# Kernel tuning notes

Hardware: AMD Instinct MI355X
Metric: run time of the kernel (lower is better)

## Reference

```python
import jax, jax.numpy as jnp
import numpy as np

EPS = 1e-5

def mlp_layer(h, W, b, g, be):
    # Linear -> BatchNorm1d (training-mode batch stats over points) -> LeakyReLU
    y = h @ W + b
    mu = jnp.mean(y, axis=0)
    var = jnp.mean((y - mu) ** 2, axis=0)
    y = (y - mu) * jax.lax.rsqrt(var + EPS) * g + be
    return jax.nn.leaky_relu(y, 0.01)

def segment_unit_norm(pos, idx, S):
    # center each segment on its centroid, scale to the unit sphere, return radius*2 as diameter
    N = pos.shape[0]
    cnt = jax.ops.segment_sum(jnp.ones((N,), pos.dtype), idx, num_segments=S)
    center = jax.ops.segment_sum(pos, idx, num_segments=S) / jnp.maximum(cnt, 1.0)[:, None]
    centered = pos - center[idx]
    r2 = jax.ops.segment_max(jnp.sum(centered * centered, axis=1), idx, num_segments=S)
    r = jnp.sqrt(jnp.maximum(r2, 0.0))  # empty segments -> -inf clamped to 0
    r_safe = jnp.where(r > 0.0, r, 1.0)
    pos_n = centered / r_safe[idx][:, None]
    diameter = 2.0 * r_safe * (cnt > 0).astype(pos.dtype)
    return pos_n, diameter, cnt

def segment_max_pool(x, idx, S, cnt):
    out = jax.ops.segment_max(x, idx, num_segments=S)
    return jnp.where((cnt > 0)[:, None], out, 0.0)

def setup_inputs() -> dict:
    key = jax.random.key(0)
    ks = jax.random.split(key, 16)
    N, S = 1000000, 10000
    Cx = 64
    loc = [Cx + 3, 128, 256]
    glo = [loc[-1] + 1, 512, 512]
    d = {
        'pos': jax.random.normal(ks[0], (N, 3), jnp.float32),
        'x': jax.random.normal(ks[1], (N, Cx), jnp.float32),
        'idx': jnp.sort(jax.random.randint(ks[2], (N,), 0, S)),
        'num_segments': S,
    }
    def lin(k, fan_in, fan_out):
        s = 1.0 / np.sqrt(fan_in)
        return jax.random.uniform(k, (fan_in, fan_out), jnp.float32, -s, s)
    # local MLP params
    d['W1'], d['b1'] = lin(ks[3], loc[0], loc[1]), jnp.zeros((loc[1],), jnp.float32)
    d['g1'], d['be1'] = jnp.ones((loc[1],), jnp.float32), jnp.zeros((loc[1],), jnp.float32)
    d['W2'], d['b2'] = lin(ks[4], loc[1], loc[2]), jnp.zeros((loc[2],), jnp.float32)
    d['g2'], d['be2'] = jnp.ones((loc[2],), jnp.float32), jnp.zeros((loc[2],), jnp.float32)
    # global MLP params
    d['GW1'], d['Gb1'] = lin(ks[5], glo[0], glo[1]), jnp.zeros((glo[1],), jnp.float32)
    d['Gg1'], d['Gbe1'] = jnp.ones((glo[1],), jnp.float32), jnp.zeros((glo[1],), jnp.float32)
    d['GW2'], d['Gb2'] = lin(ks[6], glo[1], glo[2]), jnp.zeros((glo[2],), jnp.float32)
    d['Gg2'], d['Gbe2'] = jnp.ones((glo[2],), jnp.float32), jnp.zeros((glo[2],), jnp.float32)
    return d

def reference(pos, x, idx, num_segments, W1, b1, g1, be1, W2, b2, g2, be2, GW1, Gb1, Gg1, Gbe1, GW2, Gb2, Gg2, Gbe2):
    S = num_segments
    pos_n, diameter, cnt = segment_unit_norm(pos, idx, S)
    h = jnp.concatenate([x, pos_n], axis=1)            # [N, 67]
    h = mlp_layer(h, W1, b1, g1, be1)                   # [N, 128]
    h = mlp_layer(h, W2, b2, g2, be2)                   # [N, 256]
    hg = segment_max_pool(h, idx, S, cnt)               # [S, 256]
    hg = jnp.concatenate([hg, diameter[:, None]], axis=1)  # [S, 257]
    hg = mlp_layer(hg, GW1, Gb1, Gg1, Gbe1)             # [S, 512]
    hg = mlp_layer(hg, GW2, Gb2, Gg2, Gbe2)             # [S, 512]
    return hg
```

## Files before the change

kernel.cpp:

```cpp
#include <hip/hip_runtime.h>
#include <hip/hip_fp16.h>

#define LEAKY(v) ((v) < 0.0f ? 0.01f * (v) : (v))

typedef _Float16 half8 __attribute__((ext_vector_type(8)));
typedef float f32x4 __attribute__((ext_vector_type(4)));

__device__ __forceinline__ unsigned int pkrtz(float a, float b) {
  auto h = __builtin_amdgcn_cvt_pkrtz(a, b);
  union { decltype(h) h2; unsigned int u; } c; c.h2 = h; return c.u;
}
__device__ __forceinline__ unsigned short f2h(float f) {
  union { _Float16 h; unsigned short u; } c; c.h = (_Float16)f; return c.u;
}
__device__ __forceinline__ unsigned int fkey(float f) {
  unsigned int u = __float_as_uint(f);
  return ((int)u < 0) ? ~u : (u | 0x80000000u);
}
__device__ __forceinline__ float fdec(unsigned int k) {
  return __uint_as_float((k & 0x80000000u) ? (k ^ 0x80000000u) : ~k);
}


__global__ void seg_lb_kernel(const int* __restrict__ idx, int N, int S, int* __restrict__ seg_start) {
  int s = blockIdx.x * blockDim.x + threadIdx.x;
  if (s > S) return;
  int lo = 0, hi = N;
  while (lo < hi) {
    int mid = (lo + hi) >> 1;
    if (idx[mid] < s) lo = mid + 1; else hi = mid;
  }
  seg_start[s] = lo;
}

__global__ void seg_stat_kernel(const float* __restrict__ pos, const int* __restrict__ seg_start,
                                float* __restrict__ center, float* __restrict__ invr,
                                float* __restrict__ diam) {
  int s = blockIdx.x;
  int start = seg_start[s], end = seg_start[s + 1];
  int cnt = end - start;
  int lane = threadIdx.x;
  float sx = 0.f, sy = 0.f, sz = 0.f;
  for (int i = start + lane; i < end; i += 64) {
    sx += pos[3 * i + 0]; sy += pos[3 * i + 1]; sz += pos[3 * i + 2];
  }
  for (int o = 32; o > 0; o >>= 1) {
    sx += __shfl_down(sx, o); sy += __shfl_down(sy, o); sz += __shfl_down(sz, o);
  }
  float inv_cnt = 1.0f / fmaxf((float)cnt, 1.0f);
  float cx = __shfl(sx, 0) * inv_cnt;
  float cy = __shfl(sy, 0) * inv_cnt;
  float cz = __shfl(sz, 0) * inv_cnt;
  float m2 = 0.f;
  for (int i = start + lane; i < end; i += 64) {
    float dx = pos[3 * i + 0] - cx, dy = pos[3 * i + 1] - cy, dz = pos[3 * i + 2] - cz;
    m2 = fmaxf(m2, dx * dx + dy * dy + dz * dz);
  }
  for (int o = 32; o > 0; o >>= 1) m2 = fmaxf(m2, __shfl_down(m2, o));
  if (lane == 0) {
    float r = sqrtf(fmaxf(m2, 0.f));
    float rs = (r > 0.f) ? r : 1.0f;
    center[3 * s + 0] = cx; center[3 * s + 1] = cy; center[3 * s + 2] = cz;
    invr[s] = 1.0f / rs;
    diam[s] = (cnt > 0) ? 2.0f * rs : 0.0f;
  }
}


__global__ void wconv_kernel(const float* __restrict__ W, int K, int N, unsigned short* __restrict__ Wt) {
  int i = blockIdx.x * 256 + threadIdx.x;
  if (i >= N * 16) return;
  int n = i >> 4, c = i & 15;
  union { uint4 u; unsigned short h[8]; } o;
#pragma unroll
  for (int e = 0; e < 8; ++e) {
    int k = c * 8 + e;
    float v = (k < K) ? W[(size_t)k * N + n] : 0.f;
    o.h[e] = f2h(v);
  }
  *(uint4*)&Wt[(size_t)n * 128 + c * 8] = o.u;
}


__global__ __launch_bounds__(256, 3) void gemm1_kernel(
    const float* __restrict__ x, const float* __restrict__ pos, const int* __restrict__ idx,
    const float* __restrict__ center, const float* __restrict__ invr,
    const unsigned short* __restrict__ w1t, const float* __restrict__ b1,
    unsigned short* __restrict__ y1, float* __restrict__ gsum, float* __restrict__ gsq, int M) {
  __shared__ __align__(16) unsigned short As[128 * 128];
  const int tid = threadIdx.x;
  const int row0 = blockIdx.x * 128;
  const int och = tid & 15;
  const int rr = tid >> 4;

  const int lane = tid & 63;
  const int wv = tid >> 6;
  const int wr = wv >> 1, wc = wv & 1;
  const int lr = lane & 15, lg = lane >> 4;

#pragma unroll
  for (int j = 0; j < 8; ++j) {
    int n = rr + 16 * j;
    uint4 v = *(const uint4*)&w1t[n * 128 + och * 8];
    *(uint4*)&As[n * 128 + ((och ^ (n & 7)) << 3)] = v;
  }
  __syncthreads();
  half8 b[4][3];
#pragma unroll
  for (int cf = 0; cf < 4; ++cf) {
    int n = wc * 64 + cf * 16 + lr;
#pragma unroll
    for (int ks = 0; ks < 3; ++ks) {
      int c = ks * 4 + lg;
      b[cf][ks] = *(const half8*)&As[n * 128 + ((c ^ (n & 7)) << 3)];
    }
  }
  float bb[4];
#pragma unroll
  for (int cf = 0; cf < 4; ++cf) bb[cf] = b1[wc * 64 + cf * 16 + lr];
  __syncthreads();

  for (int j = 0; j < 4; ++j) {
    int c = tid + 256 * j;
    int r = c >> 3, cc = c & 7;
    int row = row0 + r;
    uint4 o = make_uint4(0u, 0u, 0u, 0u);
    if (row < M) {
      float4 v0 = *(const float4*)&x[(size_t)row * 64 + cc * 8];
      float4 v1 = *(const float4*)&x[(size_t)row * 64 + cc * 8 + 4];
      o.x = pkrtz(v0.x, v0.y); o.y = pkrtz(v0.z, v0.w);
      o.z = pkrtz(v1.x, v1.y); o.w = pkrtz(v1.z, v1.w);
    }
    *(uint4*)&As[r * 128 + ((cc ^ (r & 7)) << 3)] = o;
  }
  if (tid < 128) {
    int r = tid, row = row0 + r;
    uint4 o = make_uint4(0u, 0u, 0u, 0u);
    if (row < M) {
      int s = idx[row];
      float ir = invr[s];
      float px = (pos[3 * row + 0] - center[3 * s + 0]) * ir;
      float py = (pos[3 * row + 1] - center[3 * s + 1]) * ir;
      float pz = (pos[3 * row + 2] - center[3 * s + 2]) * ir;
      o.x = pkrtz(px, py); o.y = pkrtz(pz, 0.f);
    }
    *(uint4*)&As[r * 128 + ((8 ^ (r & 7)) << 3)] = o;
  } else {
    int r = tid - 128;
    uint4 z = make_uint4(0u, 0u, 0u, 0u);
    *(uint4*)&As[r * 128 + ((9 ^ (r & 7)) << 3)] = z;
    *(uint4*)&As[r * 128 + ((10 ^ (r & 7)) << 3)] = z;
    *(uint4*)&As[r * 128 + ((11 ^ (r & 7)) << 3)] = z;
  }
  __syncthreads();

  const f32x4 fzero = {0.f, 0.f, 0.f, 0.f};
  f32x4 acc[4][4];
#pragma unroll
  for (int rf = 0; rf < 4; ++rf)
#pragma unroll
    for (int cf = 0; cf < 4; ++cf) acc[rf][cf] = fzero;

#pragma unroll
  for (int ks = 0; ks < 3; ++ks) {
    int c = ks * 4 + lg;
    half8 a[4];
#pragma unroll
    for (int rf = 0; rf < 4; ++rf) {
      int row = wr * 64 + rf * 16 + lr;
      a[rf] = *(const half8*)&As[row * 128 + ((c ^ (row & 7)) << 3)];
    }
#pragma unroll
    for (int cf = 0; cf < 4; ++cf)
#pragma unroll
      for (int rf = 0; rf < 4; ++rf)
        acc[rf][cf] = __builtin_amdgcn_mfma_f32_16x16x32_f16(a[rf], b[cf][ks], acc[rf][cf], 0, 0, 0);
  }

  __syncthreads();
#pragma unroll
  for (int cf = 0; cf < 4; ++cf) {
    int col = wc * 64 + cf * 16 + lr;
#pragma unroll
    for (int rf = 0; rf < 4; ++rf) {
#pragma unroll
      for (int r = 0; r < 4; ++r) {
        int row = wr * 64 + rf * 16 + lg * 4 + r;
        As[row * 128 + (((col >> 3) ^ (row & 7)) << 3) + (col & 7)] = f2h(acc[rf][cf][r] + bb[cf]);
      }
    }
  }
  __syncthreads();
  float psum[8], psq[8];
#pragma unroll
  for (int c = 0; c < 8; ++c) { psum[c] = 0.f; psq[c] = 0.f; }
  for (int j = 0; j < 8; ++j) {
    int r = rr + 16 * j;
    int row = row0 + r;
    if (row < M) {
      uint4 v = *(const uint4*)&As[r * 128 + ((och ^ (r & 7)) << 3)];
      *(uint4*)&y1[(size_t)row * 128 + och * 8] = v;
      union { uint4 u; _Float16 h[8]; } w; w.u = v;
#pragma unroll
      for (int c = 0; c < 8; ++c) { float f = (float)w.h[c]; psum[c] += f; psq[c] += f * f; }
    }
  }
  __syncthreads();
  float* redS = (float*)As;
  float* redQ = redS + 16 * 128;
#pragma unroll
  for (int c = 0; c < 8; ++c) {
    redS[rr * 128 + och * 8 + c] = psum[c];
    redQ[rr * 128 + och * 8 + c] = psq[c];
  }
  __syncthreads();
  if (tid < 128) {
    float s = 0.f, q = 0.f;
#pragma unroll
    for (int g = 0; g < 16; ++g) { s += redS[g * 128 + tid]; q += redQ[g * 128 + tid]; }
    atomicAdd(&gsum[tid], s);
    atomicAdd(&gsq[tid], q);
  }
}


__global__ __launch_bounds__(256, 2) void gemm2_kernel(
    const unsigned short* __restrict__ y1,
    const unsigned short* __restrict__ a1h, const unsigned short* __restrict__ c1h,
    const unsigned short* __restrict__ w2t, const float* __restrict__ b2,
    const int* __restrict__ idx,
    unsigned int* __restrict__ segmx, unsigned int* __restrict__ segmn,
    float* __restrict__ gsum, float* __restrict__ gsq,
    int M, int ntiles) {
  __shared__ __align__(16) unsigned short As[128 * 128];
  __shared__ __align__(16) unsigned short Bs[128 * 128];
  int* sids = (int*)Bs;
  const int tid = threadIdx.x;
  const int col0 = blockIdx.x * 128;
  const int och = tid & 15;
  const int rr = tid >> 4;
  const int tstep = gridDim.y;

  const _Float16* ap = (const _Float16*)a1h;
  const _Float16* cp = (const _Float16*)c1h;
  _Float16 av[8], cv[8];
#pragma unroll
  for (int q = 0; q < 8; ++q) { av[q] = ap[och * 8 + q]; cv[q] = cp[och * 8 + q]; }

#pragma unroll
  for (int j = 0; j < 8; ++j) {
    int n = rr + 16 * j;
    uint4 v = *(const uint4*)&w2t[(size_t)(col0 + n) * 128 + och * 8];
    *(uint4*)&Bs[n * 128 + ((och ^ (n & 7)) << 3)] = v;
  }

  int t = blockIdx.y;
  uint4 pf[8];
#pragma unroll
  for (int j = 0; j < 8; ++j) {
    int row = t * 128 + rr + 16 * j;
    pf[j] = make_uint4(0u, 0u, 0u, 0u);
    if (row < M) pf[j] = *(const uint4*)&y1[(size_t)row * 128 + och * 8];
  }
  __syncthreads();

  const int lane = tid & 63;
  const int wv = tid >> 6;
  const int wr = wv >> 1, wc = wv & 1;
  const int lr = lane & 15, lg = lane >> 4;

  half8 b[4][4];
#pragma unroll
  for (int cf = 0; cf < 4; ++cf) {
    int n = wc * 64 + cf * 16 + lr;
#pragma unroll
    for (int ks = 0; ks < 4; ++ks) {
      int c = ks * 4 + lg;
      b[cf][ks] = *(const half8*)&Bs[n * 128 + ((c ^ (n & 7)) << 3)];
    }
  }
  float bb[4];
#pragma unroll
  for (int cf = 0; cf < 4; ++cf) bb[cf] = b2[col0 + wc * 64 + cf * 16 + lr];

#pragma unroll
  for (int j = 0; j < 8; ++j) {
    int r = rr + 16 * j;
    union { uint4 u; _Float16 h[8]; } w; w.u = pf[j];
#pragma unroll
    for (int q = 0; q < 8; ++q) {
      _Float16 v = w.h[q] * av[q] + cv[q];
      w.h[q] = (v < (_Float16)0.f) ? v * (_Float16)0.01f : v;
    }
    *(uint4*)&As[r * 128 + ((och ^ (r & 7)) << 3)] = w.u;
  }
  __syncthreads();

  const int scol = tid & 127;
  const int sh = tid >> 7;
  float psumc = 0.f, psqc = 0.f;

  const f32x4 fzero = {0.f, 0.f, 0.f, 0.f};

  for (;;) {
    const int tn = t + tstep;
    const bool more = tn < ntiles;
    if (tid < 128) {
      int row = t * 128 + tid;
      sids[tid] = (row < M) ? idx[row] : -1;
    }
    if (more) {
#pragma unroll
      for (int j = 0; j < 8; ++j) {
        int row = tn * 128 + rr + 16 * j;
        pf[j] = make_uint4(0u, 0u, 0u, 0u);
        if (row < M) pf[j] = *(const uint4*)&y1[(size_t)row * 128 + och * 8];
      }
    }
    f32x4 acc[4][4];
#pragma unroll
    for (int rf = 0; rf < 4; ++rf)
#pragma unroll
      for (int cf = 0; cf < 4; ++cf) acc[rf][cf] = fzero;
#pragma unroll
    for (int ks = 0; ks < 4; ++ks) {
      half8 a[4];
      int c = ks * 4 + lg;
#pragma unroll
      for (int rf = 0; rf < 4; ++rf) {
        int row = wr * 64 + rf * 16 + lr;
        a[rf] = *(const half8*)&As[row * 128 + ((c ^ (row & 7)) << 3)];
      }
#pragma unroll
      for (int cf = 0; cf < 4; ++cf)
#pragma unroll
        for (int rf = 0; rf < 4; ++rf)
          acc[rf][cf] = __builtin_amdgcn_mfma_f32_16x16x32_f16(a[rf], b[cf][ks], acc[rf][cf], 0, 0, 0);
    }
    __syncthreads();
#pragma unroll
    for (int cf = 0; cf < 4; ++cf) {
      int col = wc * 64 + cf * 16 + lr;
#pragma unroll
      for (int rf = 0; rf < 4; ++rf) {
#pragma unroll
        for (int r = 0; r < 4; ++r) {
          int row = wr * 64 + rf * 16 + lg * 4 + r;
          As[row * 128 + (((col >> 3) ^ (row & 7)) << 3) + (col & 7)] = f2h(acc[rf][cf][r] + bb[cf]);
        }
      }
    }
    __syncthreads();
    {
      int rows = M - t * 128; if (rows > 128) rows = 128;
      int rbeg = sh * 64;
      int rend = rbeg + 64; if (rend > rows) rend = rows;
      float mx = -3.4e38f, mn = 3.4e38f;
      int cur = (rbeg < rend) ? sids[rbeg] : -1;
      for (int r = rbeg; r < rend; ++r) {
        int sgm = sids[r];
        float v = (float)*(const _Float16*)&As[r * 128 + (((scol >> 3) ^ (r & 7)) << 3) + (scol & 7)];
        if (sgm != cur) {
          atomicMax(&segmx[(size_t)cur * 256 + col0 + scol], fkey(mx));
          atomicMin(&segmn[(size_t)cur * 256 + col0 + scol], fkey(mn));
          mx = -3.4e38f; mn = 3.4e38f; cur = sgm;
        }
        mx = fmaxf(mx, v); mn = fminf(mn, v);
        psumc += v; psqc += v * v;
      }
      if (cur >= 0) {
        atomicMax(&segmx[(size_t)cur * 256 + col0 + scol], fkey(mx));
        atomicMin(&segmn[(size_t)cur * 256 + col0 + scol], fkey(mn));
      }
    }
    __syncthreads();
    if (!more) break;
#pragma unroll
    for (int j = 0; j < 8; ++j) {
      int r = rr + 16 * j;
      union { uint4 u; _Float16 h[8]; } w; w.u = pf[j];
#pragma unroll
      for (int q = 0; q < 8; ++q) {
        _Float16 v = w.h[q] * av[q] + cv[q];
        w.h[q] = (v < (_Float16)0.f) ? v * (_Float16)0.01f : v;
      }
      *(uint4*)&As[r * 128 + ((och ^ (r & 7)) << 3)] = w.u;
    }
    t = tn;
    __syncthreads();
  }

  float* red = (float*)(Bs + 512);
  if (sh) { red[scol] = psumc; red[128 + scol] = psqc; }
  __syncthreads();
  if (!sh) {
    atomicAdd(&gsum[col0 + scol], psumc + red[scol]);
    atomicAdd(&gsq[col0 + scol], psqc + red[128 + scol]);
  }
}


__device__ __forceinline__ void mm_tile(const float* __restrict__ As, const float* __restrict__ Bs,
                                        int bk, int tr, int tc, float acc[4][8]) {
  for (int k4 = 0; k4 < bk; k4 += 4) {
    float4 a[4];
#pragma unroll
    for (int r = 0; r < 4; ++r) a[r] = *(const float4*)&As[(tr * 4 + r) * 68 + k4];
#pragma unroll
    for (int kk = 0; kk < 4; ++kk) {
      float4 w0 = *(const float4*)&Bs[(k4 + kk) * 128 + tc * 8];
      float4 w1 = *(const float4*)&Bs[(k4 + kk) * 128 + tc * 8 + 4];
#pragma unroll
      for (int r = 0; r < 4; ++r) {
        float av = (kk == 0) ? a[r].x : (kk == 1) ? a[r].y : (kk == 2) ? a[r].z : a[r].w;
        acc[r][0] = fmaf(av, w0.x, acc[r][0]);
        acc[r][1] = fmaf(av, w0.y, acc[r][1]);
        acc[r][2] = fmaf(av, w0.z, acc[r][2]);
        acc[r][3] = fmaf(av, w0.w, acc[r][3]);
        acc[r][4] = fmaf(av, w1.x, acc[r][4]);
        acc[r][5] = fmaf(av, w1.y, acc[r][5]);
        acc[r][6] = fmaf(av, w1.z, acc[r][6]);
        acc[r][7] = fmaf(av, w1.w, acc[r][7]);
      }
    }
  }
}

__device__ __forceinline__ void stats_reduce(float* redS, float* redQ,
                                             const float psum[8], const float psq[8],
                                             int tr, int tc, int tid,
                                             float* __restrict__ gsum, float* __restrict__ gsq, int col0) {
  __syncthreads();
#pragma unroll
  for (int c = 0; c < 8; ++c) {
    redS[tr * 128 + tc * 8 + c] = psum[c];
    redQ[tr * 128 + tc * 8 + c] = psq[c];
  }
  __syncthreads();
  if (tid < 128) {
    float s = 0.f, q = 0.f;
#pragma unroll
    for (int r = 0; r < 16; ++r) { s += redS[r * 128 + tid]; q += redQ[r * 128 + tid]; }
    atomicAdd(&gsum[col0 + tid], s);
    atomicAdd(&gsq[col0 + tid], q);
  }
}


template <bool NORM>
__global__ __launch_bounds__(256) void gemmG_kernel(
    const float* __restrict__ A, int lda, int K, int M,
    const float* __restrict__ an, const float* __restrict__ cn,
    const float* __restrict__ W, const float* __restrict__ bias,
    float* __restrict__ Y, float* __restrict__ gsum, float* __restrict__ gsq) {
  __shared__ float As[64 * 68];
  __shared__ float Bs[64 * 128];
  const int tid = threadIdx.x;
  const int row0 = blockIdx.x * 64;
  const int col0 = blockIdx.y * 128;
  const int tr = tid >> 4, tc = tid & 15;
  float acc[4][8];
#pragma unroll
  for (int r = 0; r < 4; ++r)
#pragma unroll
    for (int c = 0; c < 8; ++c) acc[r][c] = 0.f;

  const int nkb = (K + 63) >> 6;
  for (int kb = 0; kb < nkb; ++kb) {
    if (kb) __syncthreads();
    for (int e = tid; e < 64 * 64; e += 256) {
      int r = e >> 6, c = e & 63;
      int row = row0 + r, k = kb * 64 + c;
      float v = 0.f;
      if (row < M && k < K) {
        v = A[(size_t)row * lda + k];
        if (NORM) { v = an[k] * v + cn[k]; v = LEAKY(v); }
      }
      As[r * 68 + c] = v;
    }
    for (int e = tid; e < 64 * 32; e += 256) {
      int r = e >> 5, c4 = e & 31;
      int k = kb * 64 + r;
      float4 v = make_float4(0.f, 0.f, 0.f, 0.f);
      if (k < K) v = *(const float4*)&W[(size_t)k * 512 + col0 + c4 * 4];
      *(float4*)&Bs[r * 128 + c4 * 4] = v;
    }
    __syncthreads();
    mm_tile(As, Bs, 64, tr, tc, acc);
  }

  float psum[8], psq[8];
#pragma unroll
  for (int c = 0; c < 8; ++c) { psum[c] = 0.f; psq[c] = 0.f; }
#pragma unroll
  for (int r = 0; r < 4; ++r) {
    int row = row0 + tr * 4 + r;
    if (row < M) {
      float yv[8];
#pragma unroll
      for (int c = 0; c < 8; ++c) {
        yv[c] = acc[r][c] + bias[col0 + tc * 8 + c];
        psum[c] += yv[c]; psq[c] += yv[c] * yv[c];
      }
      *(float4*)&Y[(size_t)row * 512 + col0 + tc * 8] = make_float4(yv[0], yv[1], yv[2], yv[3]);
      *(float4*)&Y[(size_t)row * 512 + col0 + tc * 8 + 4] = make_float4(yv[4], yv[5], yv[6], yv[7]);
    }
  }
  stats_reduce(As, Bs, psum, psq, tr, tc, tid, gsum, gsq, col0);
}


__global__ void finalize_kernel(const float* __restrict__ gsum, const float* __restrict__ gsq,
                                const float* __restrict__ g, const float* __restrict__ be,
                                float invn, int C, float* __restrict__ a, float* __restrict__ c,
                                unsigned short* __restrict__ ah, unsigned short* __restrict__ chh) {
  int j = blockIdx.x * blockDim.x + threadIdx.x;
  if (j >= C) return;
  float mu = gsum[j] * invn;
  float var = gsq[j] * invn - mu * mu;
  float aj = g[j] * rsqrtf(var + 1e-5f);
  float cj = be[j] - mu * aj;
  a[j] = aj;
  c[j] = cj;
  if (ah) { ah[j] = f2h(aj); chh[j] = f2h(cj); }
}


__global__ void poolfin_kernel(const unsigned int* __restrict__ segmx, const unsigned int* __restrict__ segmn,
                               const int* __restrict__ seg_start,
                               const float* __restrict__ a2, const float* __restrict__ c2,
                               const float* __restrict__ diam, float* __restrict__ hg) {
  int s = blockIdx.x;
  int j = threadIdx.x;
  bool nonempty = seg_start[s + 1] > seg_start[s];
  float aj = a2[j], cj = c2[j];
  unsigned int k = (aj >= 0.f) ? segmx[(size_t)s * 256 + j] : segmn[(size_t)s * 256 + j];
  float f = fdec(k);
  float v = aj * f + cj;
  v = LEAKY(v);
  hg[(size_t)s * 257 + j] = nonempty ? v : 0.0f;
  if (j == 0) hg[(size_t)s * 257 + 256] = diam[s];
}


__global__ void final_kernel(const float* __restrict__ y4, const float* __restrict__ a4,
                             const float* __restrict__ c4, float* __restrict__ out, int total) {
  int i = blockIdx.x * blockDim.x + threadIdx.x;
  if (i >= total) return;
  int j = i & 511;
  float v = a4[j] * y4[i] + c4[j];
  out[i] = LEAKY(v);
}


extern "C" void kernel_launch(void* const* d_in, const int* in_sizes, int n_in,
                              void* d_out, int out_size, void* d_ws, size_t ws_size,
                              hipStream_t stream) {
  const float* pos  = (const float*)d_in[0];
  const float* x    = (const float*)d_in[1];
  const int*   idx  = (const int*)d_in[2];
  const float* W1   = (const float*)d_in[4];
  const float* b1   = (const float*)d_in[5];
  const float* g1   = (const float*)d_in[6];
  const float* be1  = (const float*)d_in[7];
  const float* W2   = (const float*)d_in[8];
  const float* b2   = (const float*)d_in[9];
  const float* g2   = (const float*)d_in[10];
  const float* be2  = (const float*)d_in[11];
  const float* GW1  = (const float*)d_in[12];
  const float* Gb1  = (const float*)d_in[13];
  const float* Gg1  = (const float*)d_in[14];
  const float* Gbe1 = (const float*)d_in[15];
  const float* GW2  = (const float*)d_in[16];
  const float* Gb2  = (const float*)d_in[17];
  const float* Gg2  = (const float*)d_in[18];
  const float* Gbe2 = (const float*)d_in[19];
  float* out = (float*)d_out;

  const int N = in_sizes[0] / 3;
  const int S = 10000;

  char* ws = (char*)d_ws;
  size_t off = 0;
  auto take = [&](size_t bytes) -> char* {
    char* p = ws + off;
    off = (off + bytes + 255) & ~(size_t)255;
    return p;
  };
  int*   seg_start = (int*)take((size_t)(S + 1) * sizeof(int));
  float* center    = (float*)take((size_t)S * 3 * sizeof(float));
  float* invr      = (float*)take((size_t)S * sizeof(float));
  float* diam      = (float*)take((size_t)S * sizeof(float));
  float* stats     = (float*)take(2816 * sizeof(float));
  float* gsum1 = stats,        *gsq1 = stats + 128;
  float* gsum2 = stats + 256,  *gsq2 = stats + 512;
  float* gsum3 = stats + 768,  *gsq3 = stats + 1280;
  float* gsum4 = stats + 1792, *gsq4 = stats + 2304;
  float* par = (float*)take(2816 * sizeof(float));
  float* a1 = par,        *c1 = par + 256;
  float* a2 = par + 512,  *c2 = par + 768;
  float* a3 = par + 1024, *c3 = par + 1536;
  float* a4 = par + 2048, *c4 = par + 2560;
  unsigned short* a1h = (unsigned short*)take(128 * 2);
  unsigned short* c1h = (unsigned short*)take(128 * 2);
  unsigned short* w1t = (unsigned short*)take((size_t)128 * 128 * 2);
  unsigned short* w2t = (unsigned short*)take((size_t)256 * 128 * 2);
  float* hg = (float*)take((size_t)S * 257 * sizeof(float));
  float* y3 = (float*)take((size_t)S * 512 * sizeof(float));
  float* y4 = (float*)take((size_t)S * 512 * sizeof(float));
  unsigned int* segmx = (unsigned int*)take((size_t)S * 256 * sizeof(unsigned int));
  unsigned int* segmn = (unsigned int*)take((size_t)S * 256 * sizeof(unsigned int));
  unsigned short* y1 = (unsigned short*)take((size_t)N * 128 * 2);
  (void)ws_size; (void)n_in; (void)out_size;

  hipMemsetAsync(stats, 0, 2816 * sizeof(float), stream);
  hipMemsetAsync(segmx, 0x00, (size_t)S * 256 * sizeof(unsigned int), stream);
  hipMemsetAsync(segmn, 0xFF, (size_t)S * 256 * sizeof(unsigned int), stream);

  wconv_kernel<<<(128 * 16 + 255) / 256, 256, 0, stream>>>(W1, 67, 128, w1t);
  wconv_kernel<<<(256 * 16 + 255) / 256, 256, 0, stream>>>(W2, 128, 256, w2t);

  seg_lb_kernel<<<(S + 1 + 255) / 256, 256, 0, stream>>>(idx, N, S, seg_start);
  seg_stat_kernel<<<S, 64, 0, stream>>>(pos, seg_start, center, invr, diam);

  gemm1_kernel<<<(N + 127) / 128, 256, 0, stream>>>(x, pos, idx, center, invr, w1t, b1, y1, gsum1, gsq1, N);
  finalize_kernel<<<1, 128, 0, stream>>>(gsum1, gsq1, g1, be1, 1.0f / (float)N, 128, a1, c1, a1h, c1h);

  const int ntiles = (N + 127) / 128;
  gemm2_kernel<<<dim3(2, 256), 256, 0, stream>>>(y1, a1h, c1h, w2t, b2, idx, segmx, segmn,
                                                 gsum2, gsq2, N, ntiles);
  finalize_kernel<<<1, 256, 0, stream>>>(gsum2, gsq2, g2, be2, 1.0f / (float)N, 256, a2, c2, nullptr, nullptr);

  poolfin_kernel<<<S, 256, 0, stream>>>(segmx, segmn, seg_start, a2, c2, diam, hg);

  gemmG_kernel<false><<<dim3((S + 63) / 64, 4), 256, 0, stream>>>(hg, 257, 257, S, nullptr, nullptr,
                                                                  GW1, Gb1, y3, gsum3, gsq3);
  finalize_kernel<<<2, 256, 0, stream>>>(gsum3, gsq3, Gg1, Gbe1, 1.0f / (float)S, 512, a3, c3, nullptr, nullptr);

  gemmG_kernel<true><<<dim3((S + 63) / 64, 4), 256, 0, stream>>>(y3, 512, 512, S, a3, c3,
                                                                 GW2, Gb2, y4, gsum4, gsq4);
  finalize_kernel<<<2, 256, 0, stream>>>(gsum4, gsq4, Gg2, Gbe2, 1.0f / (float)S, 512, a4, c4, nullptr, nullptr);

  final_kernel<<<(S * 512 + 255) / 256, 256, 0, stream>>>(y4, a4, c4, out, S * 512);
}
```

Baseline: 769.7 us.

## Make gemm1 persistent with prefetch and double-buffer gemm2 output tiles

gemm1 becomes a persistent kernel on 512 blocks. Each block loops over row tiles and prefetches the next tile's x, pos and center data into registers while the MFMA work runs. It also writes results to a separate output shared buffer, and the per-block atomic statistics reduction now happens once per block instead of once per tile. gemm2 separates its A and output shared buffers and double-buffers the segment-id array, which removes two barriers per iteration. The cost is more shared memory per block, which lowers occupancy (gemm1 launch bounds go from 3 to 2), and more register pressure from the prefetch.

Result: faster. 708.9 us (-7.9%).

```diff
diff --git a/kernel.cpp b/kernel.cpp
--- a/kernel.cpp
+++ b/kernel.cpp
@@ -82,29 +82,23 @@
 }
 
 
-__global__ __launch_bounds__(256, 3) void gemm1_kernel(
+__global__ __launch_bounds__(256, 2) void gemm1_kernel(
     const float* __restrict__ x, const float* __restrict__ pos, const int* __restrict__ idx,
     const float* __restrict__ center, const float* __restrict__ invr,
     const unsigned short* __restrict__ w1t, const float* __restrict__ b1,
-    unsigned short* __restrict__ y1, float* __restrict__ gsum, float* __restrict__ gsq, int M) {
-  __shared__ __align__(16) unsigned short As[128 * 128];
+    unsigned short* __restrict__ y1, float* __restrict__ gsum, float* __restrict__ gsq,
+    int M, int ntiles) {
+  __shared__ __align__(16) unsigned short Asm[128 * 128];
+  __shared__ __align__(16) unsigned short Osm[128 * 128];
   const int tid = threadIdx.x;
-  const int row0 = blockIdx.x * 128;
   const int och = tid & 15;
   const int rr = tid >> 4;
-
   const int lane = tid & 63;
   const int wv = tid >> 6;
   const int wr = wv >> 1, wc = wv & 1;
   const int lr = lane & 15, lg = lane >> 4;
-
-#pragma unroll
-  for (int j = 0; j < 8; ++j) {
-    int n = rr + 16 * j;
-    uint4 v = *(const uint4*)&w1t[n * 128 + och * 8];
-    *(uint4*)&As[n * 128 + ((och ^ (n & 7)) << 3)] = v;
-  }
-  __syncthreads();
+  const int tstep = gridDim.x;
+
   half8 b[4][3];
 #pragma unroll
   for (int cf = 0; cf < 4; ++cf) {
@@ -112,101 +106,138 @@
 #pragma unroll
     for (int ks = 0; ks < 3; ++ks) {
       int c = ks * 4 + lg;
-      b[cf][ks] = *(const half8*)&As[n * 128 + ((c ^ (n & 7)) << 3)];
+      b[cf][ks] = *(const half8*)&w1t[n * 128 + c * 8];
     }
   }
   float bb[4];
 #pragma unroll
   for (int cf = 0; cf < 4; ++cf) bb[cf] = b1[wc * 64 + cf * 16 + lr];
-  __syncthreads();
-
-  for (int j = 0; j < 4; ++j) {
-    int c = tid + 256 * j;
-    int r = c >> 3, cc = c & 7;
-    int row = row0 + r;
-    uint4 o = make_uint4(0u, 0u, 0u, 0u);
-    if (row < M) {
-      float4 v0 = *(const float4*)&x[(size_t)row * 64 + cc * 8];
-      float4 v1 = *(const float4*)&x[(size_t)row * 64 + cc * 8 + 4];
-      o.x = pkrtz(v0.x, v0.y); o.y = pkrtz(v0.z, v0.w);
-      o.z = pkrtz(v1.x, v1.y); o.w = pkrtz(v1.z, v1.w);
-    }
-    *(uint4*)&As[r * 128 + ((cc ^ (r & 7)) << 3)] = o;
-  }
+
   if (tid < 128) {
-    int r = tid, row = row0 + r;
-    uint4 o = make_uint4(0u, 0u, 0u, 0u);
-    if (row < M) {
-      int s = idx[row];
-      float ir = invr[s];
-      float px = (pos[3 * row + 0] - center[3 * s + 0]) * ir;
-      float py = (pos[3 * row + 1] - center[3 * s + 1]) * ir;
-      float pz = (pos[3 * row + 2] - center[3 * s + 2]) * ir;
-      o.x = pkrtz(px, py); o.y = pkrtz(pz, 0.f);
-    }
-    *(uint4*)&As[r * 128 + ((8 ^ (r & 7)) << 3)] = o;
-  } else {
-    int r = tid - 128;
     uint4 z = make_uint4(0u, 0u, 0u, 0u);
-    *(uint4*)&As[r * 128 + ((9 ^ (r & 7)) << 3)] = z;
-    *(uint4*)&As[r * 128 + ((10 ^ (r & 7)) << 3)] = z;
-    *(uint4*)&As[r * 128 + ((11 ^ (r & 7)) << 3)] = z;
-  }
-  __syncthreads();
+    int r = tid;
+    *(uint4*)&Asm[r * 128 + ((9 ^ (r & 7)) << 3)] = z;
+    *(uint4*)&Asm[r * 128 + ((10 ^ (r & 7)) << 3)] = z;
+    *(uint4*)&Asm[r * 128 + ((11 ^ (r & 7)) << 3)] = z;
+  }
+
+  float4 pfx[8];
+  float pp0 = 0.f, pp1 = 0.f, pp2 = 0.f, pc0 = 0.f, pc1 = 0.f, pc2 = 0.f, pir = 0.f;
+
+  auto prefetch = [&](int tt) {
+#pragma unroll
+    for (int j = 0; j < 4; ++j) {
+      int c = tid + 256 * j;
+      int r = c >> 3, cc = c & 7;
+      int row = tt * 128 + r;
+      pfx[2 * j] = make_float4(0.f, 0.f, 0.f, 0.f);
+      pfx[2 * j + 1] = make_float4(0.f, 0.f, 0.f, 0.f);
+      if (row < M) {
+        pfx[2 * j]     = *(const float4*)&x[(size_t)row * 64 + cc * 8];
+        pfx[2 * j + 1] = *(const float4*)&x[(size_t)row * 64 + cc * 8 + 4];
+      }
+    }
+    if (tid < 128) {
+      int row = tt * 128 + tid;
+      pp0 = pp1 = pp2 = pc0 = pc1 = pc2 = 0.f; pir = 0.f;
+      if (row < M) {
+        int s = idx[row];
+        pp0 = pos[3 * row + 0]; pp1 = pos[3 * row + 1]; pp2 = pos[3 * row + 2];
+        pc0 = center[3 * s + 0]; pc1 = center[3 * s + 1]; pc2 = center[3 * s + 2];
+        pir = invr[s];
+      }
+    }
+  };
+  auto stageA = [&]() {
+#pragma unroll
+    for (int j = 0; j < 4; ++j) {
+      int c = tid + 256 * j;
+      int r = c >> 3, cc = c & 7;
+      uint4 o;
+      o.x = pkrtz(pfx[2 * j].x, pfx[2 * j].y);
+      o.y = pkrtz(pfx[2 * j].z, pfx[2 * j].w);
+      o.z = pkrtz(pfx[2 * j + 1].x, pfx[2 * j + 1].y);
+      o.w = pkrtz(pfx[2 * j + 1].z, pfx[2 * j + 1].w);
+      *(uint4*)&Asm[r * 128 + ((cc ^ (r & 7)) << 3)] = o;
+    }
+    if (tid < 128) {
+      int r = tid;
+      uint4 o = make_uint4(0u, 0u, 0u, 0u);
+      o.x = pkrtz((pp0 - pc0) * pir, (pp1 - pc1) * pir);
+      o.y = pkrtz((pp2 - pc2) * pir, 0.f);
+      *(uint4*)&Asm[r * 128 + ((8 ^ (r & 7)) << 3)] = o;
+    }
+  };
+
+  int t = blockIdx.x;
+  prefetch(t);
+  stageA();
+  __syncthreads();
+
+  float psum[8], psq[8];
+#pragma unroll
+  for (int c = 0; c < 8; ++c) { psum[c] = 0.f; psq[c] = 0.f; }
 
   const f32x4 fzero = {0.f, 0.f, 0.f, 0.f};
-  f32x4 acc[4][4];
-#pragma unroll
-  for (int rf = 0; rf < 4; ++rf)
-#pragma unroll
-    for (int cf = 0; cf < 4; ++cf) acc[rf][cf] = fzero;
-
-#pragma unroll
-  for (int ks = 0; ks < 3; ++ks) {
-    int c = ks * 4 + lg;
-    half8 a[4];
-#pragma unroll
-    for (int rf = 0; rf < 4; ++rf) {
-      int row = wr * 64 + rf * 16 + lr;
-      a[rf] = *(const half8*)&As[row * 128 + ((c ^ (row & 7)) << 3)];
-    }
-#pragma unroll
-    for (int cf = 0; cf < 4; ++cf)
-#pragma unroll
-      for (int rf = 0; rf < 4; ++rf)
-        acc[rf][cf] = __builtin_amdgcn_mfma_f32_16x16x32_f16(a[rf], b[cf][ks], acc[rf][cf], 0, 0, 0);
-  }
-
-  __syncthreads();
-#pragma unroll
-  for (int cf = 0; cf < 4; ++cf) {
-    int col = wc * 64 + cf * 16 + lr;
-#pragma unroll
-    for (int rf = 0; rf < 4; ++rf) {
-#pragma unroll
-      for (int r = 0; r < 4; ++r) {
-        int row = wr * 64 + rf * 16 + lg * 4 + r;
-        As[row * 128 + (((col >> 3) ^ (row & 7)) << 3) + (col & 7)] = f2h(acc[rf][cf][r] + bb[cf]);
-      }
-    }
-  }
-  __syncthreads();
-  float psum[8], psq[8];
-#pragma unroll
-  for (int c = 0; c < 8; ++c) { psum[c] = 0.f; psq[c] = 0.f; }
-  for (int j = 0; j < 8; ++j) {
-    int r = rr + 16 * j;
-    int row = row0 + r;
-    if (row < M) {
-      uint4 v = *(const uint4*)&As[r * 128 + ((och ^ (r & 7)) << 3)];
-      *(uint4*)&y1[(size_t)row * 128 + och * 8] = v;
-      union { uint4 u; _Float16 h[8]; } w; w.u = v;
-#pragma unroll
-      for (int c = 0; c < 8; ++c) { float f = (float)w.h[c]; psum[c] += f; psq[c] += f * f; }
-    }
-  }
-  __syncthreads();
-  float* redS = (float*)As;
+
+  for (;;) {
+    const int tn = t + tstep;
+    const bool more = tn < ntiles;
+    if (more) prefetch(tn);
+    f32x4 acc[4][4];
+#pragma unroll
+    for (int rf = 0; rf < 4; ++rf)
+#pragma unroll
+      for (int cf = 0; cf < 4; ++cf) acc[rf][cf] = fzero;
+#pragma unroll
+    for (int ks = 0; ks < 3; ++ks) {
+      half8 a[4];
+      int c = ks * 4 + lg;
+#pragma unroll
+      for (int rf = 0; rf < 4; ++rf) {
+        int row = wr * 64 + rf * 16 + lr;
+        a[rf] = *(const half8*)&Asm[row * 128 + ((c ^ (row & 7)) << 3)];
+      }
+#pragma unroll
+      for (int cf = 0; cf < 4; ++cf)
+#pragma unroll
+        for (int rf = 0; rf < 4; ++rf)
+          acc[rf][cf] = __builtin_amdgcn_mfma_f32_16x16x32_f16(a[rf], b[cf][ks], acc[rf][cf], 0, 0, 0);
+    }
+#pragma unroll
+    for (int cf = 0; cf < 4; ++cf) {
+      int col = wc * 64 + cf * 16 + lr;
+#pragma unroll
+      for (int rf = 0; rf < 4; ++rf) {
+#pragma unroll
+        for (int r = 0; r < 4; ++r) {
+          int row = wr * 64 + rf * 16 + lg * 4 + r;
+          Osm[row * 128 + (((col >> 3) ^ (row & 7)) << 3) + (col & 7)] = f2h(acc[rf][cf][r] + bb[cf]);
+        }
+      }
+    }
+    __syncthreads();
+    const int row0 = t * 128;
+#pragma unroll
+    for (int j = 0; j < 8; ++j) {
+      int r = rr + 16 * j;
+      int row = row0 + r;
+      if (row < M) {
+        uint4 v = *(const uint4*)&Osm[r * 128 + ((och ^ (r & 7)) << 3)];
+        *(uint4*)&y1[(size_t)row * 128 + och * 8] = v;
+        union { uint4 u; _Float16 h[8]; } w; w.u = v;
+#pragma unroll
+        for (int c = 0; c < 8; ++c) { float f = (float)w.h[c]; psum[c] += f; psq[c] += f * f; }
+      }
+    }
+    if (!more) break;
+    stageA();
+    t = tn;
+    __syncthreads();
+  }
+
+  __syncthreads();
+  float* redS = (float*)Osm;
   float* redQ = redS + 16 * 128;
 #pragma unroll
   for (int c = 0; c < 8; ++c) {
@@ -232,9 +263,9 @@
     unsigned int* __restrict__ segmx, unsigned int* __restrict__ segmn,
     float* __restrict__ gsum, float* __restrict__ gsq,
     int M, int ntiles) {
-  __shared__ __align__(16) unsigned short As[128 * 128];
-  __shared__ __align__(16) unsigned short Bs[128 * 128];
-  int* sids = (int*)Bs;
+  __shared__ __align__(16) unsigned short Asm[128 * 128];
+  __shared__ __align__(16) unsigned short Osm[128 * 128];
+  __shared__ int sbuf[2][128];
   const int tid = threadIdx.x;
   const int col0 = blockIdx.x * 128;
   const int och = tid & 15;
@@ -251,7 +282,7 @@
   for (int j = 0; j < 8; ++j) {
     int n = rr + 16 * j;
     uint4 v = *(const uint4*)&w2t[(size_t)(col0 + n) * 128 + och * 8];
-    *(uint4*)&Bs[n * 128 + ((och ^ (n & 7)) << 3)] = v;
+    *(uint4*)&Osm[n * 128 + ((och ^ (n & 7)) << 3)] = v;
   }
 
   int t = blockIdx.y;
@@ -262,6 +293,10 @@
     pf[j] = make_uint4(0u, 0u, 0u, 0u);
     if (row < M) pf[j] = *(const uint4*)&y1[(size_t)row * 128 + och * 8];
   }
+  if (tid < 128) {
+    int row = t * 128 + tid;
+    sbuf[0][tid] = (row < M) ? idx[row] : -1;
+  }
   __syncthreads();
 
   const int lane = tid & 63;
@@ -276,7 +311,7 @@
 #pragma unroll
     for (int ks = 0; ks < 4; ++ks) {
       int c = ks * 4 + lg;
-      b[cf][ks] = *(const half8*)&Bs[n * 128 + ((c ^ (n & 7)) << 3)];
+      b[cf][ks] = *(const half8*)&Osm[n * 128 + ((c ^ (n & 7)) << 3)];
     }
   }
   float bb[4];
@@ -292,23 +327,20 @@
       _Float16 v = w.h[q] * av[q] + cv[q];
       w.h[q] = (v < (_Float16)0.f) ? v * (_Float16)0.01f : v;
     }
-    *(uint4*)&As[r * 128 + ((och ^ (r & 7)) << 3)] = w.u;
+    *(uint4*)&Asm[r * 128 + ((och ^ (r & 7)) << 3)] = w.u;
   }
   __syncthreads();
 
   const int scol = tid & 127;
   const int sh = tid >> 7;
   float psumc = 0.f, psqc = 0.f;
+  int p = 0;
 
   const f32x4 fzero = {0.f, 0.f, 0.f, 0.f};
 
   for (;;) {
     const int tn = t + tstep;
     const bool more = tn < ntiles;
-    if (tid < 128) {
-      int row = t * 128 + tid;
-      sids[tid] = (row < M) ? idx[row] : -1;
-    }
     if (more) {
 #pragma unroll
       for (int j = 0; j < 8; ++j) {
@@ -316,6 +348,10 @@
         pf[j] = make_uint4(0u, 0u, 0u, 0u);
         if (row < M) pf[j] = *(const uint4*)&y1[(size_t)row * 128 + och * 8];
       }
+      if (tid < 128) {
+        int row = tn * 128 + tid;
+        sbuf[p ^ 1][tid] = (row < M) ? idx[row] : -1;
+      }
     }
     f32x4 acc[4][4];
 #pragma unroll
@@ -329,7 +365,7 @@
 #pragma unroll
       for (int rf = 0; rf < 4; ++rf) {
         int row = wr * 64 + rf * 16 + lr;
-        a[rf] = *(const half8*)&As[row * 128 + ((c ^ (row & 7)) << 3)];
+        a[rf] = *(const half8*)&Asm[row * 128 + ((c ^ (row & 7)) << 3)];
       }
 #pragma unroll
       for (int cf = 0; cf < 4; ++cf)
@@ -337,7 +373,6 @@
         for (int rf = 0; rf < 4; ++rf)
           acc[rf][cf] = __builtin_amdgcn_mfma_f32_16x16x32_f16(a[rf], b[cf][ks], acc[rf][cf], 0, 0, 0);
     }
-    __syncthreads();
 #pragma unroll
     for (int cf = 0; cf < 4; ++cf) {
       int col = wc * 64 + cf * 16 + lr;
@@ -346,7 +381,7 @@
 #pragma unroll
         for (int r = 0; r < 4; ++r) {
           int row = wr * 64 + rf * 16 + lg * 4 + r;
-          As[row * 128 + (((col >> 3) ^ (row & 7)) << 3) + (col & 7)] = f2h(acc[rf][cf][r] + bb[cf]);
+          Osm[row * 128 + (((col >> 3) ^ (row & 7)) << 3) + (col & 7)] = f2h(acc[rf][cf][r] + bb[cf]);
         }
       }
     }
@@ -356,10 +391,11 @@
       int rbeg = sh * 64;
       int rend = rbeg + 64; if (rend > rows) rend = rows;
       float mx = -3.4e38f, mn = 3.4e38f;
+      const int* sids = sbuf[p];
       int cur = (rbeg < rend) ? sids[rbeg] : -1;
       for (int r = rbeg; r < rend; ++r) {
         int sgm = sids[r];
-        float v = (float)*(const _Float16*)&As[r * 128 + (((scol >> 3) ^ (r & 7)) << 3) + (scol & 7)];
+        float v = (float)*(const _Float16*)&Osm[r * 128 + (((scol >> 3) ^ (r & 7)) << 3) + (scol & 7)];
         if (sgm != cur) {
           atomicMax(&segmx[(size_t)cur * 256 + col0 + scol], fkey(mx));
           atomicMin(&segmn[(size_t)cur * 256 + col0 + scol], fkey(mn));
@@ -373,7 +409,6 @@
         atomicMin(&segmn[(size_t)cur * 256 + col0 + scol], fkey(mn));
       }
     }
-    __syncthreads();
     if (!more) break;
 #pragma unroll
     for (int j = 0; j < 8; ++j) {
@@ -384,13 +419,14 @@
         _Float16 v = w.h[q] * av[q] + cv[q];
         w.h[q] = (v < (_Float16)0.f) ? v * (_Float16)0.01f : v;
       }
-      *(uint4*)&As[r * 128 + ((och ^ (r & 7)) << 3)] = w.u;
-    }
-    t = tn;
+      *(uint4*)&Asm[r * 128 + ((och ^ (r & 7)) << 3)] = w.u;
+    }
+    t = tn; p ^= 1;
     __syncthreads();
   }
 
-  float* red = (float*)(Bs + 512);
+  __syncthreads();
+  float* red = (float*)Asm;
   if (sh) { red[scol] = psumc; red[128 + scol] = psqc; }
   __syncthreads();
   if (!sh) {
@@ -623,10 +659,10 @@
   seg_lb_kernel<<<(S + 1 + 255) / 256, 256, 0, stream>>>(idx, N, S, seg_start);
   seg_stat_kernel<<<S, 64, 0, stream>>>(pos, seg_start, center, invr, diam);
 
-  gemm1_kernel<<<(N + 127) / 128, 256, 0, stream>>>(x, pos, idx, center, invr, w1t, b1, y1, gsum1, gsq1, N);
+  const int ntiles = (N + 127) / 128;
+  gemm1_kernel<<<512, 256, 0, stream>>>(x, pos, idx, center, invr, w1t, b1, y1, gsum1, gsq1, N, ntiles);
   finalize_kernel<<<1, 128, 0, stream>>>(gsum1, gsq1, g1, be1, 1.0f / (float)N, 128, a1, c1, a1h, c1h);
 
-  const int ntiles = (N + 127) / 128;
   gemm2_kernel<<<dim3(2, 256), 256, 0, stream>>>(y1, a1h, c1h, w2t, b2, idx, segmx, segmn,
                                                  gsum2, gsq2, N, ntiles);
   finalize_kernel<<<1, 256, 0, stream>>>(gsum2, gsq2, g2, be2, 1.0f / (float)N, 256, a2, c2, nullptr, nullptr);
```
